# Performance work log

Hardware: AMD Instinct MI355X
Metric: run time of the kernel (lower is better)

The kernel has to match this reference:

```python
import jax, jax.numpy as jnp
import numpy as np

B = 4        # number of point clouds (equal-sized, batch ids are sorted blocks)
K = 3        # knn_interpolate k
EPS_D = 1e-16
EPS_BN = 1e-5


def setup_inputs() -> dict:
    key = jax.random.key(0)
    ks = jax.random.split(key, 12)
    N_src, N_tgt = 2048, 8192
    C, C_skip = 256, 128
    x = jax.random.normal(ks[0], (B * N_src, C), dtype=jnp.float32)
    pos = jax.random.normal(ks[1], (B * N_src, 3), dtype=jnp.float32)
    x_skip = jax.random.normal(ks[2], (B * N_tgt, C_skip), dtype=jnp.float32)
    pos_skip = jax.random.normal(ks[3], (B * N_tgt, 3), dtype=jnp.float32)
    batch = jnp.repeat(jnp.arange(B, dtype=jnp.int64), N_src)
    batch_skip = jnp.repeat(jnp.arange(B, dtype=jnp.int64), N_tgt)
    d_in = C + C_skip  # 384
    W1 = jax.random.normal(ks[4], (d_in, 256), dtype=jnp.float32) / np.sqrt(d_in)
    b1 = jnp.zeros((256,), dtype=jnp.float32)
    g1 = jnp.ones((256,), dtype=jnp.float32)
    be1 = jnp.zeros((256,), dtype=jnp.float32)
    W2 = jax.random.normal(ks[5], (256, 256), dtype=jnp.float32) / 16.0
    b2 = jnp.zeros((256,), dtype=jnp.float32)
    g2 = jnp.ones((256,), dtype=jnp.float32)
    be2 = jnp.zeros((256,), dtype=jnp.float32)
    return dict(x=x, pos=pos, batch=batch, x_skip=x_skip, pos_skip=pos_skip,
                batch_skip=batch_skip, W1=W1, b1=b1, g1=g1, be1=be1,
                W2=W2, b2=b2, g2=g2, be2=be2)


def _knn_interpolate(x, pos, pos_skip):
    # equal-size clouds: reshape instead of per-batch masking
    C = x.shape[1]
    N = pos.shape[0] // B
    M = pos_skip.shape[0] // B
    ps = pos.reshape(B, N, 3)
    pt = pos_skip.reshape(B, M, 3)
    # squared distances [B, M, N] via |a|^2 + |b|^2 - 2ab
    d2 = (jnp.sum(pt * pt, -1)[:, :, None]
          + jnp.sum(ps * ps, -1)[:, None, :]
          - 2.0 * jnp.einsum('bmd,bnd->bmn', pt, ps))
    neg_d2, idx = jax.lax.top_k(-d2, K)            # idx: [B, M, K]
    w = 1.0 / jnp.maximum(-neg_d2, EPS_D)          # inverse squared distance
    xf = x.reshape(B, N, C)
    feats = xf[jnp.arange(B)[:, None, None], idx]  # [B, M, K, C] irregular gather
    y = jnp.sum(feats * w[..., None], axis=2) / jnp.sum(w, axis=2)[..., None]
    return y.reshape(B * M, C)


def _mlp_block(h, W, b, g, be):
    h = jnp.maximum(h @ W + b, 0.0)                # Linear + ReLU
    mu = jnp.mean(h, axis=0)
    var = jnp.mean((h - mu) ** 2, axis=0)          # biased var (torch BN training)
    return g * (h - mu) / jnp.sqrt(var + EPS_BN) + be


def reference(x, pos, batch, x_skip, pos_skip, batch_skip,
              W1, b1, g1, be1, W2, b2, g2, be2):
    y = _knn_interpolate(x, pos, pos_skip)
    h = jnp.concatenate([y, x_skip], axis=1)       # [B*M, 384]
    h = _mlp_block(h, W1, b1, g1, be1)
    h = _mlp_block(h, W2, b2, g2, be2)
    return h
```

## Files before the change

kernel.cpp:

```cpp
#include <hip/hip_runtime.h>
#include <hip/hip_bf16.h>

typedef __attribute__((ext_vector_type(8))) short short8;
typedef __attribute__((ext_vector_type(4))) int   i32x4;
typedef __attribute__((ext_vector_type(4))) float f32x4;
typedef __attribute__((ext_vector_type(2))) float f32x2;
typedef __attribute__((ext_vector_type(8))) float f32x8;

constexpr int BATCH  = 4;
constexpr int NSRC   = 2048;
constexpr int NTGT   = 8192;
constexpr int C_IN   = 256;
constexpr int C_SKIP = 128;
constexpr int DIN    = 384;
constexpr int HID    = 256;
constexpr int MROWS  = BATCH * NTGT;

constexpr int TGT_PER_BLK = 16;
constexpr int KNN_BLOCKS  = MROWS / TGT_PER_BLK;
constexpr int WT_BLOCKS   = 8;
constexpr int LDS_STRIDE  = 36;
constexpr int NPART       = 64;

__device__ __forceinline__ short f2bf(float v) {
    __hip_bfloat16 h = __float2bfloat16(v);
    return (short)__builtin_bit_cast(unsigned short, h);
}
__device__ __forceinline__ float bf2f(short s) {
    return __uint_as_float(((unsigned)(unsigned short)s) << 16);
}

__global__ __launch_bounds__(512, 2) void knn_kernel(const float* __restrict__ pos,
                                                     const float* __restrict__ pos_skip,
                                                     const float* __restrict__ W1,
                                                     __hip_bfloat16* __restrict__ W1T,
                                                     i32x4* __restrict__ idxo,
                                                     f32x4* __restrict__ wqo,
                                                     float* __restrict__ stats,
                                                     float* __restrict__ partials) {
#pragma clang fp contract(off)
    const int blk = blockIdx.x;
    if (blk >= KNN_BLOCKS) {
        const int e = blk - KNN_BLOCKS;
        if (e < WT_BLOCKS) {
            const int r  = e * 32 + (threadIdx.x >> 4);
            const int c0 = threadIdx.x & 15;
#pragma unroll
            for (int k = 0; k < DIN / 16; ++k) {
                int c = c0 + k * 16;
                W1T[(size_t)r * DIN + c] = __float2bfloat16(W1[(size_t)c * HID + r]);
            }
        } else {
            for (int i = threadIdx.x; i < 4 * HID; i += 512) stats[i] = 0.0f;
            for (int i = threadIdx.x; i < 2 * NPART * HID; i += 512) partials[i] = 0.0f;
        }
        return;
    }
    __shared__ float4 sp[NSRC];
    const int t0 = blk * TGT_PER_BLK;
    const int b  = t0 / NTGT;
    const float* ps = pos + (size_t)b * NSRC * 3;
    for (int j = threadIdx.x; j < NSRC; j += 512) {
        float X = ps[j * 3 + 0], Y = ps[j * 3 + 1], Z = ps[j * 3 + 2];
        float s2 = ((X * X) + (Y * Y)) + (Z * Z);
        sp[j] = make_float4(X, Y, Z, s2);
    }
    __syncthreads();
    const int g  = threadIdx.x >> 5;
    const int s  = threadIdx.x & 31;
    const int tr = t0 + g;
    const float px = pos_skip[tr * 3 + 0], py = pos_skip[tr * 3 + 1], pz = pos_skip[tr * 3 + 2];
    const float pt2 = ((px * px) + (py * py)) + (pz * pz);
    const f32x2 px2 = {px, px}, py2 = {py, py}, pz2 = {pz, pz}, ptv = {pt2, pt2};
    const f32x2 two = {2.0f, 2.0f};

    float dreg[64];
    float a0 = 3e38f, a1 = 3e38f, a2 = 3e38f;
#pragma unroll
    for (int k = 0; k < NSRC / 64; ++k) {
        const int j1 = k * 64 + s;
        const int j2 = j1 + 32;
        float4 sa = sp[j1];
        float4 sb = sp[j2];
        f32x2 vx = {sa.x, sb.x}, vy = {sa.y, sb.y}, vz = {sa.z, sb.z}, vw = {sa.w, sb.w};
        f32x2 dot = ((px2 * vx) + (py2 * vy)) + (pz2 * vz);
        f32x2 d2v = (ptv + vw) - (two * dot);
        dreg[2 * k]     = d2v.x;
        dreg[2 * k + 1] = d2v.y;
#pragma unroll
        for (int h = 0; h < 2; ++h) {
            float d = h == 0 ? d2v.x : d2v.y;
            float n0 = fminf(a0, d);
            float n1 = __builtin_amdgcn_fmed3f(a0, a1, d);
            float n2 = fminf(a2, fmaxf(a1, d));
            a0 = n0; a1 = n1; a2 = n2;
        }
    }
#pragma unroll
    for (int m = 1; m <= 16; m <<= 1) {
        float oa = __shfl_xor(a0, m), ob = __shfl_xor(a1, m), oc = __shfl_xor(a2, m);
        float minb = fminf(a1, ob);
        float maxa = fmaxf(a0, oa);
        float maxb = fmaxf(a1, ob);
        float minc = fminf(a2, oc);
        float n0 = fminf(a0, oa);
        float n1 = __builtin_amdgcn_fmed3f(a0, oa, minb);
        float n2 = __builtin_amdgcn_fmed3f(minb, maxa, fminf(maxb, minc));
        a0 = n0; a1 = n1; a2 = n2;
    }

    float bd0 = 3e38f, bd1 = 3e38f, bd2 = 3e38f;
    int   bi0 = 0x7fffffff, bi1 = 0x7fffffff, bi2 = 0x7fffffff;
#pragma unroll
    for (int i = 0; i < 64; ++i) {
        float d2 = dreg[i];
        if (__any(d2 <= a2)) {
            const int j = (i >> 1) * 64 + ((i & 1) << 5) + s;
            bool c0 = d2 < bd0, c1 = d2 < bd1, c2 = d2 < bd2;
            bd2 = c1 ? bd1 : (c2 ? d2 : bd2);  bi2 = c1 ? bi1 : (c2 ? j : bi2);
            bd1 = c0 ? bd0 : (c1 ? d2 : bd1);  bi1 = c0 ? bi0 : (c1 ? j : bi1);
            bd0 = c0 ? d2  : bd0;              bi0 = c0 ? j  : bi0;
        }
    }
#pragma unroll
    for (int m = 1; m <= 16; m <<= 1) {
        float od0 = __shfl_xor(bd0, m), od1 = __shfl_xor(bd1, m), od2 = __shfl_xor(bd2, m);
        int   oi0 = __shfl_xor(bi0, m), oi1 = __shfl_xor(bi1, m), oi2 = __shfl_xor(bi2, m);
#pragma unroll
        for (int e = 0; e < 3; ++e) {
            float d = e == 0 ? od0 : (e == 1 ? od1 : od2);
            int   i = e == 0 ? oi0 : (e == 1 ? oi1 : oi2);
            bool c0 = (d < bd0) || (d == bd0 && i < bi0);
            bool c1 = (d < bd1) || (d == bd1 && i < bi1);
            bool c2 = (d < bd2) || (d == bd2 && i < bi2);
            bd2 = c1 ? bd1 : (c2 ? d : bd2);  bi2 = c1 ? bi1 : (c2 ? i : bi2);
            bd1 = c0 ? bd0 : (c1 ? d : bd1);  bi1 = c0 ? bi0 : (c1 ? i : bi1);
            bd0 = c0 ? d   : bd0;             bi0 = c0 ? i  : bi0;
        }
    }
    if (s == 0) {
        float w0 = 1.0f / fmaxf(bd0, 1e-16f);
        float w1 = 1.0f / fmaxf(bd1, 1e-16f);
        float w2 = 1.0f / fmaxf(bd2, 1e-16f);
        float inv = 1.0f / ((w0 + w1) + w2);
        idxo[tr] = i32x4{bi0, bi1, bi2, 0};
        wqo[tr]  = f32x4{w0 * inv, w1 * inv, w2 * inv, 0.0f};
    }
}

__global__ __launch_bounds__(256, 1) void zs_kernel(const float* __restrict__ x,
                                                    const float* __restrict__ xs,
                                                    const __hip_bfloat16* __restrict__ W1T,
                                                    __hip_bfloat16* __restrict__ Z,
                                                    __hip_bfloat16* __restrict__ S) {
    __shared__ short As[128 * LDS_STRIDE];
    const int blk = blockIdx.x;
    const float* A;
    __hip_bfloat16* out;
    int K, koff, m0;
    if (blk < 64) { A = x;  out = Z; K = 256; koff = 0;   m0 = blk * 128; }
    else          { A = xs; out = S; K = 128; koff = 256; m0 = (blk - 64) * 128; }
    const int t = threadIdx.x;
    const int wid = t >> 6, lane = t & 63;
    const int wr = wid & 1, wcq = wid >> 1;
    const int l15 = lane & 15, l4 = lane >> 4;
    const int arow = t >> 1, ac16 = (t & 1) * 16;
    const short* Wsh = (const short*)W1T;
    f32x4 acc[4][8] = {};
    for (int kt = 0; kt < K / 32; ++kt) {
        const float* src = A + (size_t)(m0 + arow) * K + kt * 32 + ac16;
        float4 f0 = *(const float4*)(src);
        float4 f1 = *(const float4*)(src + 4);
        float4 f2 = *(const float4*)(src + 8);
        float4 f3 = *(const float4*)(src + 12);
        short8 s0 = {f2bf(f0.x), f2bf(f0.y), f2bf(f0.z), f2bf(f0.w),
                     f2bf(f1.x), f2bf(f1.y), f2bf(f1.z), f2bf(f1.w)};
        short8 s1 = {f2bf(f2.x), f2bf(f2.y), f2bf(f2.z), f2bf(f2.w),
                     f2bf(f3.x), f2bf(f3.y), f2bf(f3.z), f2bf(f3.w)};
        __syncthreads();
        *(short8*)(&As[arow * LDS_STRIDE + ac16])     = s0;
        *(short8*)(&As[arow * LDS_STRIDE + ac16 + 8]) = s1;
        __syncthreads();
        short8 af[4], bfr[8];
#pragma unroll
        for (int mi = 0; mi < 4; ++mi)
            af[mi] = *(const short8*)(&As[(wr * 64 + mi * 16 + l15) * LDS_STRIDE + l4 * 8]);
#pragma unroll
        for (int ni = 0; ni < 8; ++ni)
            bfr[ni] = *(const short8*)(Wsh + (size_t)(wcq * 128 + ni * 16 + l15) * DIN + koff + kt * 32 + l4 * 8);
#pragma unroll
        for (int mi = 0; mi < 4; ++mi)
#pragma unroll
            for (int ni = 0; ni < 8; ++ni)
                acc[mi][ni] = __builtin_amdgcn_mfma_f32_16x16x32_bf16(af[mi], bfr[ni], acc[mi][ni], 0, 0, 0);
    }
#pragma unroll
    for (int mi = 0; mi < 4; ++mi)
#pragma unroll
        for (int r = 0; r < 4; ++r) {
            int rowg = m0 + wr * 64 + mi * 16 + l4 * 4 + r;
#pragma unroll
            for (int ni = 0; ni < 8; ++ni) {
                int col = wcq * 128 + ni * 16 + l15;
                out[(size_t)rowg * HID + col] = __float2bfloat16(acc[mi][ni][r]);
            }
        }
}

__global__ __launch_bounds__(256) void interp_kernel(const __hip_bfloat16* __restrict__ Z,
                                                     const __hip_bfloat16* __restrict__ S,
                                                     const i32x4* __restrict__ idxo,
                                                     const f32x4* __restrict__ wqo,
                                                     const float* __restrict__ b1,
                                                     __hip_bfloat16* __restrict__ H1,
                                                     float* __restrict__ partials) {
    __shared__ float ls[8][HID], lq[8][HID];
    const int t = blockIdx.x * 256 + threadIdx.x;
    const int r = t >> 5;
    const int c = (t & 31) * 8;
    i32x4 id = idxo[r];
    f32x4 wq = wqo[r];
    const int zb = (r >> 13) << 11;
    const short* Zs = (const short*)Z;
    short8 z0 = *(const short8*)(Zs + (size_t)(zb + id.x) * HID + c);
    short8 z1 = *(const short8*)(Zs + (size_t)(zb + id.y) * HID + c);
    short8 z2 = *(const short8*)(Zs + (size_t)(zb + id.z) * HID + c);
    short8 sv = *(const short8*)((const short*)S + (size_t)r * HID + c);
    f32x4 b0 = *(const f32x4*)(b1 + c);
    f32x4 b4 = *(const f32x4*)(b1 + c + 4);
    short8 ho;
    f32x8 hv;
#pragma unroll
    for (int e = 0; e < 8; ++e) {
        float bb = e < 4 ? b0[e & 3] : b4[e & 3];
        float v = wq.x * bf2f(z0[e]) + wq.y * bf2f(z1[e]) + wq.z * bf2f(z2[e])
                  + bf2f(sv[e]) + bb;
        v = fmaxf(v, 0.0f);
        hv[e] = v;
        ho[e] = f2bf(v);
    }
    *(short8*)((short*)H1 + (size_t)r * HID + c) = ho;
    const int grp = threadIdx.x >> 5;
#pragma unroll
    for (int e = 0; e < 8; ++e) {
        ls[grp][c + e] = hv[e];
        lq[grp][c + e] = hv[e] * hv[e];
    }
    __syncthreads();
    const int tc = threadIdx.x;
    float s_ = 0.0f, q_ = 0.0f;
#pragma unroll
    for (int g2 = 0; g2 < 8; ++g2) { s_ += ls[g2][tc]; q_ += lq[g2][tc]; }
    float* pS = partials + (size_t)(blockIdx.x & (NPART - 1)) * HID;
    float* pQ = partials + (size_t)NPART * HID + (size_t)(blockIdx.x & (NPART - 1)) * HID;
    atomicAdd(&pS[tc], s_);
    atomicAdd(&pQ[tc], q_);
}

__global__ __launch_bounds__(256) void foldw2_kernel(const float* __restrict__ W2,
                                                     const float* __restrict__ b2,
                                                     const float* __restrict__ partials,
                                                     const float* __restrict__ g1,
                                                     const float* __restrict__ be1,
                                                     __hip_bfloat16* __restrict__ W2T,
                                                     float* __restrict__ bias2f) {
    __shared__ float red[256];
    const int n = blockIdx.x, k = threadIdx.x;
    float sm = 0.0f, qq = 0.0f;
#pragma unroll
    for (int p = 0; p < NPART; ++p) {
        sm += partials[(size_t)p * HID + k];
        qq += partials[(size_t)NPART * HID + (size_t)p * HID + k];
    }
    float mu  = sm * (1.0f / MROWS);
    float var = qq * (1.0f / MROWS) - mu * mu;
    float scv = g1[k] / sqrtf(var + 1e-5f);
    float shv = be1[k] - mu * scv;
    float v = W2[(size_t)k * HID + n];
    W2T[(size_t)n * HID + k] = __float2bfloat16(scv * v);
    red[k] = shv * v;
    __syncthreads();
    for (int s = 128; s > 0; s >>= 1) {
        if (k < s) red[k] += red[k + s];
        __syncthreads();
    }
    if (k == 0) bias2f[n] = b2[n] + red[0];
}

template <int K>
__global__ __launch_bounds__(256, 1) void gemm_kernel(const __hip_bfloat16* __restrict__ A,
                                                      const __hip_bfloat16* __restrict__ WT,
                                                      const float* __restrict__ bias,
                                                      __hip_bfloat16* __restrict__ outp,
                                                      float* __restrict__ colsum,
                                                      float* __restrict__ colsq) {
    __shared__ short As[128 * LDS_STRIDE];
    const int t = threadIdx.x;
    const int m0 = blockIdx.x * 128;
    const int wid = t >> 6, lane = t & 63;
    const int wr = wid & 1, wcq = wid >> 1;
    const int l15 = lane & 15, l4 = lane >> 4;
    const int arow = t >> 1, acol8 = (t & 1) * 8;
    f32x4 acc[4][8] = {};
    const short* Ash = (const short*)A;
    const short* Wsh = (const short*)WT;
    for (int kt = 0; kt < K / 32; ++kt) {
        short8 v0 = *(const short8*)(Ash + (size_t)(m0 + arow) * K + kt * 32 + acol8);
        short8 v1 = *(const short8*)(Ash + (size_t)(m0 + arow) * K + kt * 32 + acol8 + 16);
        __syncthreads();
        *(short8*)(&As[arow * LDS_STRIDE + acol8]) = v0;
        *(short8*)(&As[arow * LDS_STRIDE + acol8 + 16]) = v1;
        __syncthreads();
        short8 af[4], bfr[8];
#pragma unroll
        for (int mi = 0; mi < 4; ++mi)
            af[mi] = *(const short8*)(&As[(wr * 64 + mi * 16 + l15) * LDS_STRIDE + l4 * 8]);
#pragma unroll
        for (int ni = 0; ni < 8; ++ni)
            bfr[ni] = *(const short8*)(Wsh + (size_t)(wcq * 128 + ni * 16 + l15) * K + kt * 32 + l4 * 8);
#pragma unroll
        for (int mi = 0; mi < 4; ++mi)
#pragma unroll
            for (int ni = 0; ni < 8; ++ni)
                acc[mi][ni] = __builtin_amdgcn_mfma_f32_16x16x32_bf16(af[mi], bfr[ni], acc[mi][ni], 0, 0, 0);
    }
    float bv[8];
    int col[8];
#pragma unroll
    for (int ni = 0; ni < 8; ++ni) {
        col[ni] = wcq * 128 + ni * 16 + l15;
        bv[ni] = bias[col[ni]];
    }
    float csum[8] = {}, csq[8] = {};
#pragma unroll
    for (int mi = 0; mi < 4; ++mi) {
#pragma unroll
        for (int r = 0; r < 4; ++r) {
            int rowg = m0 + wr * 64 + mi * 16 + l4 * 4 + r;
#pragma unroll
            for (int ni = 0; ni < 8; ++ni) {
                float v = fmaxf(acc[mi][ni][r] + bv[ni], 0.0f);
                outp[(size_t)rowg * HID + col[ni]] = __float2bfloat16(v);
                csum[ni] += v;
                csq[ni] += v * v;
            }
        }
    }
#pragma unroll
    for (int ni = 0; ni < 8; ++ni) {
        float sv = csum[ni], q = csq[ni];
        sv += __shfl_xor(sv, 16); sv += __shfl_xor(sv, 32);
        q  += __shfl_xor(q, 16);  q  += __shfl_xor(q, 32);
        if (l4 == 0) {
            atomicAdd(&colsum[col[ni]], sv);
            atomicAdd(&colsq[col[ni]], q);
        }
    }
}

__global__ __launch_bounds__(256) void bn2_kernel(const __hip_bfloat16* __restrict__ h2,
                                                  const float* __restrict__ sum2,
                                                  const float* __restrict__ sq2,
                                                  const float* __restrict__ g2,
                                                  const float* __restrict__ be2,
                                                  float* __restrict__ out) {
    __shared__ float lsc[HID], lsh[HID];
    {
        int c = threadIdx.x;
        float mu  = sum2[c] * (1.0f / MROWS);
        float var = sq2[c] * (1.0f / MROWS) - mu * mu;
        float scv = g2[c] / sqrtf(var + 1e-5f);
        lsc[c] = scv;
        lsh[c] = be2[c] - mu * scv;
    }
    __syncthreads();
    int idx = blockIdx.x * blockDim.x + threadIdx.x;
    const int total = MROWS * HID / 8;
    for (; idx < total; idx += gridDim.x * blockDim.x) {
        short8 v = *(const short8*)(h2 + (size_t)idx * 8);
        int c = (idx * 8) & (HID - 1);
        f32x8 o;
#pragma unroll
        for (int e = 0; e < 8; ++e) {
            float f = bf2f(v[e]);
            o[e] = lsc[c + e] * f + lsh[c + e];
        }
        *(f32x8*)(out + (size_t)idx * 8) = o;
    }
}

extern "C" void kernel_launch(void* const* d_in, const int* in_sizes, int n_in,
                              void* d_out, int out_size, void* d_ws, size_t ws_size,
                              hipStream_t stream) {
    const float* x    = (const float*)d_in[0];
    const float* pos  = (const float*)d_in[1];
    const float* xs   = (const float*)d_in[3];
    const float* poss = (const float*)d_in[4];
    const float* W1   = (const float*)d_in[6];
    const float* b1   = (const float*)d_in[7];
    const float* g1   = (const float*)d_in[8];
    const float* be1  = (const float*)d_in[9];
    const float* W2   = (const float*)d_in[10];
    const float* b2   = (const float*)d_in[11];
    const float* g2   = (const float*)d_in[12];
    const float* be2  = (const float*)d_in[13];

    char* ws = (char*)d_ws;
    size_t off = 0;
    auto alloc = [&](size_t bytes) -> void* {
        void* p = ws + off;
        off += (bytes + 255) & ~(size_t)255;
        return p;
    };
    __hip_bfloat16* W1T   = (__hip_bfloat16*)alloc((size_t)HID * DIN * 2);
    __hip_bfloat16* W2T   = (__hip_bfloat16*)alloc((size_t)HID * HID * 2);
    float*          stats = (float*)alloc(4 * HID * sizeof(float));
    float *sum2 = stats + 2 * HID, *sq2 = stats + 3 * HID;
    float*          partials = (float*)alloc(2 * NPART * HID * sizeof(float));
    float*          bias2f = (float*)alloc(HID * sizeof(float));
    i32x4*          idxo  = (i32x4*)alloc((size_t)MROWS * 16);
    f32x4*          wqo   = (f32x4*)alloc((size_t)MROWS * 16);
    __hip_bfloat16* Z     = (__hip_bfloat16*)alloc((size_t)BATCH * NSRC * HID * 2);
    __hip_bfloat16* S     = (__hip_bfloat16*)alloc((size_t)MROWS * HID * 2);
    __hip_bfloat16* H1    = (__hip_bfloat16*)alloc((size_t)MROWS * HID * 2);
    __hip_bfloat16* H2    = S;

    knn_kernel<<<KNN_BLOCKS + WT_BLOCKS + 1, 512, 0, stream>>>(pos, poss, W1, W1T, idxo, wqo,
                                                               stats, partials);
    zs_kernel<<<64 + MROWS / 128, 256, 0, stream>>>(x, xs, W1T, Z, S);
    interp_kernel<<<MROWS * 32 / 256, 256, 0, stream>>>(Z, S, idxo, wqo, b1, H1, partials);
    foldw2_kernel<<<HID, 256, 0, stream>>>(W2, b2, partials, g1, be1, W2T, bias2f);
    gemm_kernel<HID><<<MROWS / 128, 256, 0, stream>>>(H1, W2T, bias2f, H2, sum2, sq2);
    bn2_kernel<<<1024, 256, 0, stream>>>(H2, sum2, sq2, g2, be2, (float*)d_out);
}
```

Baseline: 126.9 us.

## Fuse KNN search and first-layer GEMM into one launch for overlap

Result: slower. 138.4 us (+9.1%).

```diff
diff --git a/kernel.cpp b/kernel.cpp
--- a/kernel.cpp
+++ b/kernel.cpp
@@ -18,7 +18,7 @@
 
 constexpr int TGT_PER_BLK = 16;
 constexpr int KNN_BLOCKS  = MROWS / TGT_PER_BLK;
-constexpr int WT_BLOCKS   = 8;
+constexpr int ZS_BLOCKS   = 64 + MROWS / 128;
 constexpr int LDS_STRIDE  = 36;
 constexpr int NPART       = 64;
 
@@ -30,40 +30,94 @@
     return __uint_as_float(((unsigned)(unsigned short)s) << 16);
 }
 
-__global__ __launch_bounds__(512, 2) void knn_kernel(const float* __restrict__ pos,
-                                                     const float* __restrict__ pos_skip,
-                                                     const float* __restrict__ W1,
-                                                     __hip_bfloat16* __restrict__ W1T,
-                                                     i32x4* __restrict__ idxo,
-                                                     f32x4* __restrict__ wqo,
-                                                     float* __restrict__ stats,
-                                                     float* __restrict__ partials) {
+__global__ __launch_bounds__(512) void w1t_kernel(const float* __restrict__ W1,
+                                                  __hip_bfloat16* __restrict__ W1T,
+                                                  float* __restrict__ stats,
+                                                  float* __restrict__ partials) {
+    const int e = blockIdx.x;
+    if (e < 8) {
+        const int r  = e * 32 + (threadIdx.x >> 4);
+        const int c0 = threadIdx.x & 15;
+#pragma unroll
+        for (int k = 0; k < DIN / 16; ++k) {
+            int c = c0 + k * 16;
+            W1T[(size_t)r * DIN + c] = __float2bfloat16(W1[(size_t)c * HID + r]);
+        }
+    } else {
+        for (int i = threadIdx.x; i < 4 * HID; i += 512) stats[i] = 0.0f;
+        for (int i = threadIdx.x; i < 2 * NPART * HID; i += 512) partials[i] = 0.0f;
+    }
+}
+
+__global__ __launch_bounds__(512, 2) void knn_zs_kernel(const float* __restrict__ pos,
+                                                        const float* __restrict__ pos_skip,
+                                                        const float* __restrict__ x,
+                                                        const float* __restrict__ xs,
+                                                        const __hip_bfloat16* __restrict__ W1T,
+                                                        i32x4* __restrict__ idxo,
+                                                        f32x4* __restrict__ wqo,
+                                                        __hip_bfloat16* __restrict__ Z,
+                                                        __hip_bfloat16* __restrict__ S) {
 #pragma clang fp contract(off)
+    __shared__ float4 sp[NSRC];
     const int blk = blockIdx.x;
     if (blk >= KNN_BLOCKS) {
-        const int e = blk - KNN_BLOCKS;
-        if (e < WT_BLOCKS) {
-            const int r  = e * 32 + (threadIdx.x >> 4);
-            const int c0 = threadIdx.x & 15;
-#pragma unroll
-            for (int k = 0; k < DIN / 16; ++k) {
-                int c = c0 + k * 16;
-                W1T[(size_t)r * DIN + c] = __float2bfloat16(W1[(size_t)c * HID + r]);
+        short* As = (short*)sp;
+        const int zblk = blk - KNN_BLOCKS;
+        const float* A;
+        __hip_bfloat16* out;
+        int K, koff, m0;
+        if (zblk < 64) { A = x;  out = Z; K = 256; koff = 0;   m0 = zblk * 128; }
+        else           { A = xs; out = S; K = 128; koff = 256; m0 = (zblk - 64) * 128; }
+        const int t = threadIdx.x;
+        const int wid = t >> 6, lane = t & 63;
+        const int wr = wid & 3, wcq = wid >> 2;
+        const int l15 = lane & 15, l4 = lane >> 4;
+        const int arow = t >> 2, ac8 = (t & 3) * 8;
+        const short* Wsh = (const short*)W1T;
+        f32x4 acc[2][8] = {};
+        for (int kt = 0; kt < K / 32; ++kt) {
+            const float* src = A + (size_t)(m0 + arow) * K + kt * 32 + ac8;
+            float4 f0 = *(const float4*)(src);
+            float4 f1 = *(const float4*)(src + 4);
+            short8 s0 = {f2bf(f0.x), f2bf(f0.y), f2bf(f0.z), f2bf(f0.w),
+                         f2bf(f1.x), f2bf(f1.y), f2bf(f1.z), f2bf(f1.w)};
+            __syncthreads();
+            *(short8*)(&As[arow * LDS_STRIDE + ac8]) = s0;
+            __syncthreads();
+            short8 af[2], bfr[8];
+#pragma unroll
+            for (int mi = 0; mi < 2; ++mi)
+                af[mi] = *(const short8*)(&As[(wr * 32 + mi * 16 + l15) * LDS_STRIDE + l4 * 8]);
+#pragma unroll
+            for (int ni = 0; ni < 8; ++ni)
+                bfr[ni] = *(const short8*)(Wsh + (size_t)(wcq * 128 + ni * 16 + l15) * DIN + koff + kt * 32 + l4 * 8);
+#pragma unroll
+            for (int mi = 0; mi < 2; ++mi)
+#pragma unroll
+                for (int ni = 0; ni < 8; ++ni)
+                    acc[mi][ni] = __builtin_amdgcn_mfma_f32_16x16x32_bf16(af[mi], bfr[ni], acc[mi][ni], 0, 0, 0);
+        }
+#pragma unroll
+        for (int mi = 0; mi < 2; ++mi)
+#pragma unroll
+            for (int r = 0; r < 4; ++r) {
+                int rowg = m0 + wr * 32 + mi * 16 + l4 * 4 + r;
+#pragma unroll
+                for (int ni = 0; ni < 8; ++ni) {
+                    int col = wcq * 128 + ni * 16 + l15;
+                    out[(size_t)rowg * HID + col] = __float2bfloat16(acc[mi][ni][r]);
+                }
             }
-        } else {
-            for (int i = threadIdx.x; i < 4 * HID; i += 512) stats[i] = 0.0f;
-            for (int i = threadIdx.x; i < 2 * NPART * HID; i += 512) partials[i] = 0.0f;
-        }
         return;
     }
-    __shared__ float4 sp[NSRC];
     const int t0 = blk * TGT_PER_BLK;
     const int b  = t0 / NTGT;
     const float* ps = pos + (size_t)b * NSRC * 3;
     for (int j = threadIdx.x; j < NSRC; j += 512) {
-        float X = ps[j * 3 + 0], Y = ps[j * 3 + 1], Z = ps[j * 3 + 2];
-        float s2 = ((X * X) + (Y * Y)) + (Z * Z);
-        sp[j] = make_float4(X, Y, Z, s2);
+        float X = ps[j * 3 + 0], Y = ps[j * 3 + 1], Zp = ps[j * 3 + 2];
+        float s2 = ((X * X) + (Y * Y)) + (Zp * Zp);
+        sp[j] = make_float4(X, Y, Zp, s2);
     }
     __syncthreads();
     const int g  = threadIdx.x >> 5;
@@ -146,65 +200,6 @@
         idxo[tr] = i32x4{bi0, bi1, bi2, 0};
         wqo[tr]  = f32x4{w0 * inv, w1 * inv, w2 * inv, 0.0f};
     }
-}
-
-__global__ __launch_bounds__(256, 1) void zs_kernel(const float* __restrict__ x,
-                                                    const float* __restrict__ xs,
-                                                    const __hip_bfloat16* __restrict__ W1T,
-                                                    __hip_bfloat16* __restrict__ Z,
-                                                    __hip_bfloat16* __restrict__ S) {
-    __shared__ short As[128 * LDS_STRIDE];
-    const int blk = blockIdx.x;
-    const float* A;
-    __hip_bfloat16* out;
-    int K, koff, m0;
-    if (blk < 64) { A = x;  out = Z; K = 256; koff = 0;   m0 = blk * 128; }
-    else          { A = xs; out = S; K = 128; koff = 256; m0 = (blk - 64) * 128; }
-    const int t = threadIdx.x;
-    const int wid = t >> 6, lane = t & 63;
-    const int wr = wid & 1, wcq = wid >> 1;
-    const int l15 = lane & 15, l4 = lane >> 4;
-    const int arow = t >> 1, ac16 = (t & 1) * 16;
-    const short* Wsh = (const short*)W1T;
-    f32x4 acc[4][8] = {};
-    for (int kt = 0; kt < K / 32; ++kt) {
-        const float* src = A + (size_t)(m0 + arow) * K + kt * 32 + ac16;
-        float4 f0 = *(const float4*)(src);
-        float4 f1 = *(const float4*)(src + 4);
-        float4 f2 = *(const float4*)(src + 8);
-        float4 f3 = *(const float4*)(src + 12);
-        short8 s0 = {f2bf(f0.x), f2bf(f0.y), f2bf(f0.z), f2bf(f0.w),
-                     f2bf(f1.x), f2bf(f1.y), f2bf(f1.z), f2bf(f1.w)};
-        short8 s1 = {f2bf(f2.x), f2bf(f2.y), f2bf(f2.z), f2bf(f2.w),
-                     f2bf(f3.x), f2bf(f3.y), f2bf(f3.z), f2bf(f3.w)};
-        __syncthreads();
-        *(short8*)(&As[arow * LDS_STRIDE + ac16])     = s0;
-        *(short8*)(&As[arow * LDS_STRIDE + ac16 + 8]) = s1;
-        __syncthreads();
-        short8 af[4], bfr[8];
-#pragma unroll
-        for (int mi = 0; mi < 4; ++mi)
-            af[mi] = *(const short8*)(&As[(wr * 64 + mi * 16 + l15) * LDS_STRIDE + l4 * 8]);
-#pragma unroll
-        for (int ni = 0; ni < 8; ++ni)
-            bfr[ni] = *(const short8*)(Wsh + (size_t)(wcq * 128 + ni * 16 + l15) * DIN + koff + kt * 32 + l4 * 8);
-#pragma unroll
-        for (int mi = 0; mi < 4; ++mi)
-#pragma unroll
-            for (int ni = 0; ni < 8; ++ni)
-                acc[mi][ni] = __builtin_amdgcn_mfma_f32_16x16x32_bf16(af[mi], bfr[ni], acc[mi][ni], 0, 0, 0);
-    }
-#pragma unroll
-    for (int mi = 0; mi < 4; ++mi)
-#pragma unroll
-        for (int r = 0; r < 4; ++r) {
-            int rowg = m0 + wr * 64 + mi * 16 + l4 * 4 + r;
-#pragma unroll
-            for (int ni = 0; ni < 8; ++ni) {
-                int col = wcq * 128 + ni * 16 + l15;
-                out[(size_t)rowg * HID + col] = __float2bfloat16(acc[mi][ni][r]);
-            }
-        }
 }
 
 __global__ __launch_bounds__(256) void interp_kernel(const __hip_bfloat16* __restrict__ Z,
@@ -425,9 +420,9 @@
     __hip_bfloat16* H1    = (__hip_bfloat16*)alloc((size_t)MROWS * HID * 2);
     __hip_bfloat16* H2    = S;
 
-    knn_kernel<<<KNN_BLOCKS + WT_BLOCKS + 1, 512, 0, stream>>>(pos, poss, W1, W1T, idxo, wqo,
-                                                               stats, partials);
-    zs_kernel<<<64 + MROWS / 128, 256, 0, stream>>>(x, xs, W1T, Z, S);
+    w1t_kernel<<<9, 512, 0, stream>>>(W1, W1T, stats, partials);
+    knn_zs_kernel<<<KNN_BLOCKS + ZS_BLOCKS, 512, 0, stream>>>(pos, poss, x, xs, W1T,
+                                                              idxo, wqo, Z, S);
     interp_kernel<<<MROWS * 32 / 256, 256, 0, stream>>>(Z, S, idxo, wqo, b1, H1, partials);
     foldw2_kernel<<<HID, 256, 0, stream>>>(W2, b2, partials, g1, be1, W2T, bias2f);
     gemm_kernel<HID><<<MROWS / 128, 256, 0, stream>>>(H1, W2T, bias2f, H2, sum2, sq2);
```
